# Optimization experiments

Hardware: AMD Instinct MI355X
Metric: run time of the kernel (lower is better)

## Reference

```python
import jax, jax.numpy as jnp
import numpy as np

B, T, C, H = 512, 256, 512, 4
HS = C // H          # head_size = 128
FF = 4 * C           # ffn_fanout * n_embd = 2048
NF = 2               # n_ffn dual FFN branches
EPS = 1e-8


def setup_inputs() -> dict:
    key = jax.random.key(0)
    ks = jax.random.split(key, 12)
    s = 0.02
    return {
        "x": jax.random.normal(ks[0], (B, T, C), jnp.float32),
        "Wq": jax.random.normal(ks[1], (H, C, HS), jnp.float32) * s,
        "Wk": jax.random.normal(ks[2], (H, C, HS), jnp.float32) * s,
        "bk": jax.random.normal(ks[3], (H, HS), jnp.float32) * s,
        "Wv": jax.random.normal(ks[4], (H, C, HS), jnp.float32) * s,
        "Wproj": jax.random.normal(ks[5], (C, C), jnp.float32) * s,
        "bproj": jax.random.normal(ks[6], (C,), jnp.float32) * s,
        "w1": jnp.ones((1,), jnp.float32),
        "w2": jnp.ones((1,), jnp.float32),
        "Wi": jax.random.normal(ks[7], (NF, C, FF), jnp.float32) * s,
        "Wo": jax.random.normal(ks[8], (NF, FF, C), jnp.float32) * s,
    }


def _rmsnorm(v, w):
    # MyNorm: scalar weight * x * rsqrt(mean(x^2, -1) + eps)
    return w * v * jax.lax.rsqrt(jnp.mean(v * v, axis=-1, keepdims=True) + EPS)


def reference(x, Wq, Wk, bk, Wv, Wproj, bproj, w1, w2, Wi, Wo):
    Bc, Tc, Cc = x.shape
    h = _rmsnorm(x, w1)
    # per-head projections (key has bias; query/value do not)
    q = jnp.einsum("btc,hcd->bhtd", h, Wq)
    k = jnp.einsum("btc,hcd->bhtd", h, Wk) + bk[None, :, None, :]
    v = jnp.einsum("btc,hcd->bhtd", h, Wv)
    # NOTE: original scales by full channel dim C**-0.5, not head_size
    scale = Cc ** (-0.5)
    wei = jnp.einsum("bhtd,bhsd->bhts", q, k) * scale
    causal = jnp.tril(jnp.ones((Tc, Tc), bool))
    wei = jnp.where(causal[None, None], wei, -jnp.inf)
    wei = jax.nn.softmax(wei, axis=-1)  # dropout: identity (inference)
    attn = jnp.einsum("bhts,bhsd->bhtd", wei, v)
    attn = attn.transpose(0, 2, 1, 3).reshape(Bc, Tc, Cc)
    x = x + attn @ Wproj + bproj  # dropout before proj: identity
    x = _rmsnorm(x, w2)
    # dual-branch FFN, averaged (exact GELU, as torch nn.GELU default)
    hmid = jax.nn.gelu(jnp.einsum("btc,ncf->nbtf", x, Wi), approximate=False)
    ff = jnp.mean(jnp.einsum("nbtf,nfc->nbtc", hmid, Wo), axis=0)
    return x + ff
```

## Files before the change

### kernel.cpp

```cpp
#include <hip/hip_runtime.h>
#include <cstdint>
#include <cstddef>

#define TOKENS 131072
#define B_BATCH 512
#define T_SEQ 256
#define C_DIM 512
#define H_HEADS 4
#define HS_DIM 128
#define FF_DIM 2048
#define EPS_RMS 1e-8f
#define SM_SCALE 0.044194173824159216f

typedef short bf16x8 __attribute__((ext_vector_type(8)));
typedef float f32x4 __attribute__((ext_vector_type(4)));
typedef unsigned short ushort_t;

__device__ __forceinline__ ushort_t f2bf(float f) {
    uint32_t u = __builtin_bit_cast(uint32_t, f);
    u += 0x7FFFu + ((u >> 16) & 1u);
    return (ushort_t)(u >> 16);
}

__device__ __forceinline__ float bf2f(ushort_t u) {
    return __builtin_bit_cast(float, (uint32_t)u << 16);
}

__device__ __forceinline__ float gelu_f(float x) {
    float u = 0.7978845608028654f * x + 0.035677408136300125f * (x * x * x);
    float e = __expf(2.0f * u);
    float t = 1.0f - 2.0f / (1.0f + e);
    return 0.5f * x * (1.0f + t);
}

__device__ __forceinline__ void stage8k(ushort_t* lds, const ushort_t* g) {
    __builtin_amdgcn_global_load_lds(
        (const __attribute__((address_space(1))) uint32_t*)g,
        (__attribute__((address_space(3))) uint32_t*)lds,
        16, 0, 0);
}

__global__ void prep_qkv(const float* __restrict__ Wq, const float* __restrict__ Wk,
                         const float* __restrict__ Wv, ushort_t* __restrict__ WqkvT) {
    int idx = blockIdx.x * 256 + threadIdx.x;
    if (idx >= 1536 * 512) return;
    int n = idx >> 9;
    int k = idx & 511;
    int h = (n & 511) >> 7;
    int d = n & 127;
    float v;
    size_t s = ((size_t)h * 512 + k) * 128 + d;
    if (n < 512)       v = Wq[s];
    else if (n < 1024) v = Wk[s];
    else               v = Wv[s];
    WqkvT[idx] = f2bf(v);
}

__global__ void prep_bias(const float* __restrict__ bk, float* __restrict__ bias1536) {
    int n = blockIdx.x * 256 + threadIdx.x;
    if (n >= 1536) return;
    bias1536[n] = (n >= 512 && n < 1024) ? bk[n - 512] : 0.0f;
}

__global__ void prep_proj(const float* __restrict__ Wproj, ushort_t* __restrict__ WprojT) {
    int idx = blockIdx.x * 256 + threadIdx.x;
    if (idx >= 512 * 512) return;
    int n = idx >> 9, k = idx & 511;
    WprojT[idx] = f2bf(Wproj[(size_t)k * 512 + n]);
}

__global__ void prep_wi(const float* __restrict__ Wi, ushort_t* __restrict__ WiT) {
    int idx = blockIdx.x * 256 + threadIdx.x;
    if (idx >= 2 * 2048 * 512) return;
    int b = idx >> 20;
    int rem = idx & 1048575;
    int f = rem >> 9, c = rem & 511;
    WiT[idx] = f2bf(Wi[((size_t)b * 512 + c) * 2048 + f]);
}

__global__ void prep_wo(const float* __restrict__ Wo, ushort_t* __restrict__ WoT2) {
    int idx = blockIdx.x * 256 + threadIdx.x;
    if (idx >= 512 * 4096) return;
    int c  = idx >> 12;
    int n2 = idx & 4095;
    int br = n2 >> 11;
    int f  = n2 & 2047;
    WoT2[idx] = f2bf(0.5f * Wo[(((size_t)br * 2048 + f) * 512) + c]);
}

__global__ __launch_bounds__(256) void rmsnorm_kernel(const float* __restrict__ in,
                                                      const float* __restrict__ wptr,
                                                      ushort_t* __restrict__ outb) {
    const int lane = threadIdx.x & 63;
    const int wave = threadIdx.x >> 6;
    const size_t token = (size_t)blockIdx.x * 4 + wave;
    const float* row = in + token * 512;
    float4 v0 = *(const float4*)(row + lane * 8);
    float4 v1 = *(const float4*)(row + lane * 8 + 4);
    float ss = v0.x*v0.x + v0.y*v0.y + v0.z*v0.z + v0.w*v0.w
             + v1.x*v1.x + v1.y*v1.y + v1.z*v1.z + v1.w*v1.w;
    #pragma unroll
    for (int d = 32; d; d >>= 1) ss += __shfl_xor(ss, d);
    float scale = wptr[0] * rsqrtf(ss * (1.0f / 512.0f) + EPS_RMS);
    float vals[8] = {v0.x, v0.y, v0.z, v0.w, v1.x, v1.y, v1.z, v1.w};
    union { ushort_t us[8]; uint4 u4; } pk;
    #pragma unroll
    for (int i = 0; i < 8; i++) pk.us[i] = f2bf(vals[i] * scale);
    *(uint4*)(outb + token * 512 + lane * 8) = pk.u4;
}

template<int MODE>
__global__ __launch_bounds__(512) void gemm256(
    const ushort_t* __restrict__ A, const ushort_t* __restrict__ Bt,
    float* Cf, ushort_t* __restrict__ Cb,
    const float* __restrict__ bias, const float* __restrict__ X,
    const ushort_t* __restrict__ Xb,
    int N, int K)
{
    __shared__ __align__(16) ushort_t S[2][2][256 * 64];
    const int tid  = threadIdx.x;
    const int lane = tid & 63;
    const int wave = tid >> 6;
    const int wm = wave >> 2;
    const int wn = wave & 3;

    const int nwg  = (int)gridDim.x;
    const int orig = (int)blockIdx.x;
    const int wgid = (orig & 7) * (nwg >> 3) + (orig >> 3);
    const int gx   = N >> 8;
    const int bm = (wgid / gx) << 8;
    const int bn = (wgid % gx) << 8;

    const int NT = K >> 6;

    const int sx = (((lane & 7) ^ (lane >> 3)) << 3);

    auto stA = [&](int dbuf, int part, int ts) {
        int tc = ts < NT ? ts : NT - 1;
        #pragma unroll
        for (int i = 0; i < 2; i++) {
            int rbase = i * 128 + part * 64 + wave * 8;
            stage8k(&S[dbuf][0][rbase * 64],
                    A + (size_t)(bm + rbase + (lane >> 3)) * K + tc * 64 + sx);
        }
    };
    auto stB = [&](int dbuf, int part, int ts) {
        int tc = ts < NT ? ts : NT - 1;
        #pragma unroll
        for (int i = 0; i < 2; i++) {
            int rbase = i * 128 + (wave >> 2) * 64 + part * 32 + (wave & 3) * 8;
            stage8k(&S[dbuf][1][rbase * 64],
                    Bt + (size_t)(bn + rbase + (lane >> 3)) * K + tc * 64 + sx);
        }
    };

    const int r16 = lane & 15;
    const int l7  = lane & 7;
    const int q   = lane >> 4;
    const int ge0 = ((q)     ^ l7) << 3;
    const int ge1 = ((4 + q) ^ l7) << 3;

    f32x4 acc[8][4] = {};
    bf16x8 a[4][2], bA[2][2], bB[2][2];

#define LDA(BUF, MH) { _Pragma("unroll") for (int mf = 0; mf < 4; mf++) { \
    int R = wm * 128 + (MH) * 64 + mf * 16 + r16; \
    a[mf][0] = *(const bf16x8*)&S[BUF][0][R * 64 + ge0]; \
    a[mf][1] = *(const bf16x8*)&S[BUF][0][R * 64 + ge1]; } }
#define LDB(BUF, NH, breg) { _Pragma("unroll") for (int nf = 0; nf < 2; nf++) { \
    int R = wn * 64 + (NH) * 32 + nf * 16 + r16; \
    breg[nf][0] = *(const bf16x8*)&S[BUF][1][R * 64 + ge0]; \
    breg[nf][1] = *(const bf16x8*)&S[BUF][1][R * 64 + ge1]; } }
#define MM(MH, NH, breg) { __builtin_amdgcn_s_setprio(1); \
    _Pragma("unroll") for (int mf = 0; mf < 4; mf++) \
    _Pragma("unroll") for (int nf = 0; nf < 2; nf++) { \
        f32x4 t0 = __builtin_amdgcn_mfma_f32_16x16x32_bf16(a[mf][0], breg[nf][0], acc[(MH)*4+mf][(NH)*2+nf], 0, 0, 0); \
        acc[(MH)*4+mf][(NH)*2+nf] = __builtin_amdgcn_mfma_f32_16x16x32_bf16(a[mf][1], breg[nf][1], t0, 0, 0, 0); } \
    __builtin_amdgcn_s_setprio(0); }
#define BAR    __builtin_amdgcn_s_barrier()
#define WAITL  { asm volatile("s_waitcnt lgkmcnt(0)" ::: "memory"); __builtin_amdgcn_sched_barrier(0); }
#define WAITLV { asm volatile("s_waitcnt lgkmcnt(0)\n\ts_waitcnt vmcnt(6)" ::: "memory"); __builtin_amdgcn_sched_barrier(0); }

    stA(0, 0, 0); stB(0, 0, 0); stB(0, 1, 0); stA(0, 1, 0);
    stA(1, 0, 1); stB(1, 0, 1); stB(1, 1, 1);
    asm volatile("s_waitcnt vmcnt(6)" ::: "memory");
    __builtin_amdgcn_sched_barrier(0);
    BAR;

    const int NI = NT >> 1;
    for (int I = 0; I < NI; ++I) {
        const int t = 2 * I;
        LDA(0, 0); LDB(0, 0, bA);  stA(1, 1, t + 1);  BAR; WAITL;  MM(0, 0, bA); BAR;
        LDB(0, 1, bB);             stA(0, 0, t + 2);  BAR; WAITL;  MM(0, 1, bB); BAR;
        LDA(0, 1);                 stB(0, 0, t + 2);  BAR; WAITL;  MM(1, 1, bB); BAR;
                                   stB(0, 1, t + 2);  BAR; WAITLV; MM(1, 0, bA); BAR;
        LDA(1, 0); LDB(1, 0, bA);  stA(0, 1, t + 2);  BAR; WAITL;  MM(0, 0, bA); BAR;
        LDB(1, 1, bB);             stA(1, 0, t + 3);  BAR; WAITL;  MM(0, 1, bB); BAR;
        LDA(1, 1);                 stB(1, 0, t + 3);  BAR; WAITL;  MM(1, 1, bB); BAR;
                                   stB(1, 1, t + 3);  BAR; WAITLV; MM(1, 0, bA); BAR;
    }
#undef LDA
#undef LDB
#undef MM
#undef BAR
#undef WAITL
#undef WAITLV

    #pragma unroll
    for (int mf = 0; mf < 8; mf++) {
        #pragma unroll
        for (int nf = 0; nf < 4; nf++) {
            #pragma unroll
            for (int j = 0; j < 4; j++) {
                int r = bm + wm * 128 + mf * 16 + (lane >> 4) * 4 + j;
                int c = bn + wn * 64 + nf * 16 + r16;
                float v = acc[mf][nf][j];
                size_t idx = (size_t)r * N + c;
                if (MODE == 0)      { Cb[idx] = f2bf(v + bias[c]); }
                else if (MODE == 1) { Cf[idx] = v + bias[c] + X[idx]; }
                else if (MODE == 2) { Cb[idx] = f2bf(gelu_f(v)); }
                else                { Cf[idx] = bf2f(Xb[idx]) + v; }
            }
        }
    }
}

__global__ __launch_bounds__(256) void attn_kernel(const ushort_t* __restrict__ QKV,
                                                   ushort_t* __restrict__ Ao) {
    __shared__ __align__(16) ushort_t Ks[32 * 136];
    __shared__ __align__(16) ushort_t VsT[128 * 40];
    __shared__ __align__(16) ushort_t Ps[4][16 * 40];
    const int tid  = threadIdx.x;
    const int lane = tid & 63;
    const int wave = tid >> 6;
    const int qtile = blockIdx.x;
    const int bh = blockIdx.y;
    const int b = bh >> 2;
    const int h = bh & 3;
    const int qb = qtile * 64;
    const int q0 = qb + wave * 16;
    const size_t baseTok = (size_t)b * T_SEQ;

    bf16x8 qf[4];
    {
        const ushort_t* qrow = QKV + (baseTok + q0 + (lane & 15)) * 1536 + h * 128 + (lane >> 4) * 8;
        #pragma unroll
        for (int dc = 0; dc < 4; dc++)
            qf[dc] = *(const bf16x8*)(qrow + dc * 32);
    }

    float m_run[4], l_run[4];
    f32x4 o[8];
    #pragma unroll
    for (int j = 0; j < 4; j++) { m_run[j] = -INFINITY; l_run[j] = 0.0f; }
    #pragma unroll
    for (int nt = 0; nt < 8; nt++) o[nt] = f32x4{0.f, 0.f, 0.f, 0.f};

    const int nchunks = qtile * 2 + 2;
    for (int kc = 0; kc < nchunks; kc++) {
        const int kbase = kc * 32;
        __syncthreads();
        #pragma unroll
        for (int r = 0; r < 2; r++) {
            int li = r * 256 + tid;
            int row = li >> 4;
            int c8 = (li & 15) * 8;
            size_t g = (baseTok + kbase + row) * 1536;
            uint4 vk = *(const uint4*)(QKV + g + 512 + h * 128 + c8);
            *(uint4*)(&Ks[row * 136 + c8]) = vk;
            uint4 vv = *(const uint4*)(QKV + g + 1024 + h * 128 + c8);
            ushort_t* pv = (ushort_t*)&vv;
            #pragma unroll
            for (int jj = 0; jj < 8; jj++)
                VsT[(c8 + jj) * 40 + row] = pv[jj];
        }
        __syncthreads();

        if (q0 + 15 >= kbase) {
            f32x4 s0 = {0.f,0.f,0.f,0.f}, s1 = {0.f,0.f,0.f,0.f};
            #pragma unroll
            for (int dc = 0; dc < 4; dc++) {
                bf16x8 kf0 = *(const bf16x8*)(&Ks[(lane & 15) * 136 + dc * 32 + (lane >> 4) * 8]);
                bf16x8 kf1 = *(const bf16x8*)(&Ks[(16 + (lane & 15)) * 136 + dc * 32 + (lane >> 4) * 8]);
                s0 = __builtin_amdgcn_mfma_f32_16x16x32_bf16(qf[dc], kf0, s0, 0, 0, 0);
                s1 = __builtin_amdgcn_mfma_f32_16x16x32_bf16(qf[dc], kf1, s1, 0, 0, 0);
            }
            const int key0 = kbase + (lane & 15);
            const int key1 = key0 + 16;
            float p0[4], p1[4], alpha[4];
            #pragma unroll
            for (int j = 0; j < 4; j++) {
                int qrow = q0 + (lane >> 4) * 4 + j;
                float sv0 = (key0 <= qrow) ? s0[j] * SM_SCALE : -INFINITY;
                float sv1 = (key1 <= qrow) ? s1[j] * SM_SCALE : -INFINITY;
                float mx = fmaxf(sv0, sv1);
                #pragma unroll
                for (int d = 1; d < 16; d <<= 1) mx = fmaxf(mx, __shfl_xor(mx, d));
                float mnew = fmaxf(m_run[j], mx);
                float aa = expf(m_run[j] - mnew);
                p0[j] = expf(sv0 - mnew);
                p1[j] = expf(sv1 - mnew);
                float rs = p0[j] + p1[j];
                #pragma unroll
                for (int d = 1; d < 16; d <<= 1) rs += __shfl_xor(rs, d);
                l_run[j] = l_run[j] * aa + rs;
                m_run[j] = mnew;
                alpha[j] = aa;
            }
            #pragma unroll
            for (int nt = 0; nt < 8; nt++)
                #pragma unroll
                for (int j = 0; j < 4; j++) o[nt][j] *= alpha[j];
            #pragma unroll
            for (int j = 0; j < 4; j++) {
                int rloc = (lane >> 4) * 4 + j;
                Ps[wave][rloc * 40 + (lane & 15)]      = f2bf(p0[j]);
                Ps[wave][rloc * 40 + 16 + (lane & 15)] = f2bf(p1[j]);
            }
            bf16x8 pa = *(const bf16x8*)(&Ps[wave][(lane & 15) * 40 + (lane >> 4) * 8]);
            #pragma unroll
            for (int nt = 0; nt < 8; nt++) {
                bf16x8 vf = *(const bf16x8*)(&VsT[(nt * 16 + (lane & 15)) * 40 + (lane >> 4) * 8]);
                o[nt] = __builtin_amdgcn_mfma_f32_16x16x32_bf16(pa, vf, o[nt], 0, 0, 0);
            }
        }
    }

    #pragma unroll
    for (int j = 0; j < 4; j++) {
        float inv = 1.0f / l_run[j];
        size_t row = baseTok + q0 + (lane >> 4) * 4 + j;
        #pragma unroll
        for (int nt = 0; nt < 8; nt++)
            Ao[row * 512 + h * 128 + nt * 16 + (lane & 15)] = f2bf(o[nt][j] * inv);
    }
}

extern "C" void kernel_launch(void* const* d_in, const int* in_sizes, int n_in,
                              void* d_out, int out_size, void* d_ws, size_t ws_size,
                              hipStream_t stream) {
    const float* x     = (const float*)d_in[0];
    const float* Wq    = (const float*)d_in[1];
    const float* Wk    = (const float*)d_in[2];
    const float* bk    = (const float*)d_in[3];
    const float* Wv    = (const float*)d_in[4];
    const float* Wproj = (const float*)d_in[5];
    const float* bproj = (const float*)d_in[6];
    const float* w1    = (const float*)d_in[7];
    const float* w2    = (const float*)d_in[8];
    const float* Wi    = (const float*)d_in[9];
    const float* Wo    = (const float*)d_in[10];
    float* out = (float*)d_out;
    (void)in_sizes; (void)n_in; (void)out_size;

    char* ws = (char*)d_ws;
    size_t off = 0;
    auto alloc = [&](size_t bytes) -> void* {
        void* p = ws + off;
        off += (bytes + 255) & ~(size_t)255;
        return p;
    };
    ushort_t* WqkvT    = (ushort_t*)alloc((size_t)1536 * 512 * 2);
    float*    bias1536 = (float*)   alloc((size_t)1536 * 4);
    ushort_t* WprojT   = (ushort_t*)alloc((size_t)512 * 512 * 2);
    ushort_t* WiT      = (ushort_t*)alloc((size_t)4096 * 512 * 2);
    ushort_t* WoT2     = (ushort_t*)alloc((size_t)512 * 4096 * 2);
    const size_t weightBytes = off;

    int nchunks = 1;
    while (nchunks < 64) {
        size_t Mc = (size_t)TOKENS / nchunks;
        size_t need = weightBytes + Mc * 512 * 2 + Mc * 4096 * 2 + 4096;
        if (need <= ws_size) break;
        nchunks *= 2;
    }
    const size_t Mc = (size_t)TOKENS / nchunks;
    const int    nbChunk = B_BATCH / nchunks;

    ushort_t* hb  = (ushort_t*)alloc(Mc * 512 * 2);
    ushort_t* big = (ushort_t*)alloc(Mc * 4096 * 2);

    prep_qkv <<<(1536 * 512 + 255) / 256, 256, 0, stream>>>(Wq, Wk, Wv, WqkvT);
    prep_bias<<<6, 256, 0, stream>>>(bk, bias1536);
    prep_proj<<<1024, 256, 0, stream>>>(Wproj, WprojT);
    prep_wi  <<<8192, 256, 0, stream>>>(Wi, WiT);
    prep_wo  <<<8192, 256, 0, stream>>>(Wo, WoT2);

    for (int ck = 0; ck < nchunks; ck++) {
        const size_t t0 = (size_t)ck * Mc;
        const float* xC   = x + t0 * 512;
        float*       zC   = out + t0 * 512;
        const int    Mi   = (int)Mc;
        const int    mt   = Mi / 256;

        rmsnorm_kernel<<<Mi / 4, 256, 0, stream>>>(xC, w1, hb);
        gemm256<0><<<mt * 6, 512, 0, stream>>>(
            hb, WqkvT, nullptr, big, bias1536, nullptr, nullptr, 1536, 512);
        attn_kernel<<<dim3(T_SEQ / 64, nbChunk * H_HEADS), 256, 0, stream>>>(big, hb);
        gemm256<1><<<mt * 2, 512, 0, stream>>>(
            hb, WprojT, zC, nullptr, bproj, xC, nullptr, 512, 512);
        rmsnorm_kernel<<<Mi / 4, 256, 0, stream>>>(zC, w2, hb);
        gemm256<2><<<mt * 16, 512, 0, stream>>>(
            hb, WiT, nullptr, big, nullptr, nullptr, nullptr, 4096, 512);
        gemm256<3><<<mt * 2, 512, 0, stream>>>(
            big, WoT2, zC, nullptr, nullptr, nullptr, hb, 512, 4096);
    }
}
```

Baseline: 2.479 ms.

## Replace 256x256 ping-pong GEMM with 128x128 triple-buffered GEMM

Swaps the 512-thread 256x256 tile GEMM, which used a hand-interleaved double-buffered schedule, for a 256-thread 128x128 tile kernel with K-step 32 and a three-stage LDS ring buffer. The grids are doubled or quadrupled to match. The simpler pipeline keeps two stages in flight and adds more workgroups, which may improve occupancy and load balance. The cost is lower arithmetic intensity per tile, more global traffic, and one barrier per K-step.

Measured after the change: 2.967 ms. 1.2x slower.

```diff
diff --git a/kernel.cpp b/kernel.cpp
--- a/kernel.cpp
+++ b/kernel.cpp
@@ -110,109 +110,88 @@
 }
 
 template<int MODE>
-__global__ __launch_bounds__(512) void gemm256(
+__global__ __launch_bounds__(256) void gemm128(
     const ushort_t* __restrict__ A, const ushort_t* __restrict__ Bt,
     float* Cf, ushort_t* __restrict__ Cb,
     const float* __restrict__ bias, const float* __restrict__ X,
     const ushort_t* __restrict__ Xb,
     int N, int K)
 {
-    __shared__ __align__(16) ushort_t S[2][2][256 * 64];
+    __shared__ __align__(16) ushort_t S[3][2][128 * 32];
     const int tid  = threadIdx.x;
     const int lane = tid & 63;
     const int wave = tid >> 6;
-    const int wm = wave >> 2;
-    const int wn = wave & 3;
+    const int wm = wave >> 1;
+    const int wn = wave & 1;
 
     const int nwg  = (int)gridDim.x;
     const int orig = (int)blockIdx.x;
     const int wgid = (orig & 7) * (nwg >> 3) + (orig >> 3);
-    const int gx   = N >> 8;
-    const int bm = (wgid / gx) << 8;
-    const int bn = (wgid % gx) << 8;
-
-    const int NT = K >> 6;
-
-    const int sx = (((lane & 7) ^ (lane >> 3)) << 3);
-
-    auto stA = [&](int dbuf, int part, int ts) {
+    const int gx   = N >> 7;
+    const int bm = (wgid / gx) << 7;
+    const int bn = (wgid % gx) << 7;
+
+    const int NT = K >> 5;
+
+    const int srcg = (((lane & 3) ^ ((lane >> 4) & 3)) << 3);
+
+    auto stage = [&](int sb, int ts) {
         int tc = ts < NT ? ts : NT - 1;
+        const int ko = tc << 5;
         #pragma unroll
         for (int i = 0; i < 2; i++) {
-            int rbase = i * 128 + part * 64 + wave * 8;
-            stage8k(&S[dbuf][0][rbase * 64],
-                    A + (size_t)(bm + rbase + (lane >> 3)) * K + tc * 64 + sx);
+            const int rb = (wave * 2 + i) * 16;
+            stage8k(&S[sb][0][rb * 32],
+                    A + (size_t)(bm + rb + (lane >> 2)) * K + ko + srcg);
+            stage8k(&S[sb][1][rb * 32],
+                    Bt + (size_t)(bn + rb + (lane >> 2)) * K + ko + srcg);
         }
     };
-    auto stB = [&](int dbuf, int part, int ts) {
-        int tc = ts < NT ? ts : NT - 1;
-        #pragma unroll
-        for (int i = 0; i < 2; i++) {
-            int rbase = i * 128 + (wave >> 2) * 64 + part * 32 + (wave & 3) * 8;
-            stage8k(&S[dbuf][1][rbase * 64],
-                    Bt + (size_t)(bn + rbase + (lane >> 3)) * K + tc * 64 + sx);
-        }
-    };
 
     const int r16 = lane & 15;
-    const int l7  = lane & 7;
     const int q   = lane >> 4;
-    const int ge0 = ((q)     ^ l7) << 3;
-    const int ge1 = ((4 + q) ^ l7) << 3;
-
-    f32x4 acc[8][4] = {};
-    bf16x8 a[4][2], bA[2][2], bB[2][2];
-
-#define LDA(BUF, MH) { _Pragma("unroll") for (int mf = 0; mf < 4; mf++) { \
-    int R = wm * 128 + (MH) * 64 + mf * 16 + r16; \
-    a[mf][0] = *(const bf16x8*)&S[BUF][0][R * 64 + ge0]; \
-    a[mf][1] = *(const bf16x8*)&S[BUF][0][R * 64 + ge1]; } }
-#define LDB(BUF, NH, breg) { _Pragma("unroll") for (int nf = 0; nf < 2; nf++) { \
-    int R = wn * 64 + (NH) * 32 + nf * 16 + r16; \
-    breg[nf][0] = *(const bf16x8*)&S[BUF][1][R * 64 + ge0]; \
-    breg[nf][1] = *(const bf16x8*)&S[BUF][1][R * 64 + ge1]; } }
-#define MM(MH, NH, breg) { __builtin_amdgcn_s_setprio(1); \
-    _Pragma("unroll") for (int mf = 0; mf < 4; mf++) \
-    _Pragma("unroll") for (int nf = 0; nf < 2; nf++) { \
-        f32x4 t0 = __builtin_amdgcn_mfma_f32_16x16x32_bf16(a[mf][0], breg[nf][0], acc[(MH)*4+mf][(NH)*2+nf], 0, 0, 0); \
-        acc[(MH)*4+mf][(NH)*2+nf] = __builtin_amdgcn_mfma_f32_16x16x32_bf16(a[mf][1], breg[nf][1], t0, 0, 0, 0); } \
-    __builtin_amdgcn_s_setprio(0); }
-#define BAR    __builtin_amdgcn_s_barrier()
-#define WAITL  { asm volatile("s_waitcnt lgkmcnt(0)" ::: "memory"); __builtin_amdgcn_sched_barrier(0); }
-#define WAITLV { asm volatile("s_waitcnt lgkmcnt(0)\n\ts_waitcnt vmcnt(6)" ::: "memory"); __builtin_amdgcn_sched_barrier(0); }
-
-    stA(0, 0, 0); stB(0, 0, 0); stB(0, 1, 0); stA(0, 1, 0);
-    stA(1, 0, 1); stB(1, 0, 1); stB(1, 1, 1);
-    asm volatile("s_waitcnt vmcnt(6)" ::: "memory");
-    __builtin_amdgcn_sched_barrier(0);
-    BAR;
-
-    const int NI = NT >> 1;
-    for (int I = 0; I < NI; ++I) {
-        const int t = 2 * I;
-        LDA(0, 0); LDB(0, 0, bA);  stA(1, 1, t + 1);  BAR; WAITL;  MM(0, 0, bA); BAR;
-        LDB(0, 1, bB);             stA(0, 0, t + 2);  BAR; WAITL;  MM(0, 1, bB); BAR;
-        LDA(0, 1);                 stB(0, 0, t + 2);  BAR; WAITL;  MM(1, 1, bB); BAR;
-                                   stB(0, 1, t + 2);  BAR; WAITLV; MM(1, 0, bA); BAR;
-        LDA(1, 0); LDB(1, 0, bA);  stA(0, 1, t + 2);  BAR; WAITL;  MM(0, 0, bA); BAR;
-        LDB(1, 1, bB);             stA(1, 0, t + 3);  BAR; WAITL;  MM(0, 1, bB); BAR;
-        LDA(1, 1);                 stB(1, 0, t + 3);  BAR; WAITL;  MM(1, 1, bB); BAR;
-                                   stB(1, 1, t + 3);  BAR; WAITLV; MM(1, 0, bA); BAR;
-    }
-#undef LDA
-#undef LDB
-#undef MM
-#undef BAR
-#undef WAITL
-#undef WAITLV
-
-    #pragma unroll
-    for (int mf = 0; mf < 8; mf++) {
+    const int ge  = ((q ^ ((r16 >> 2) & 3)) << 3);
+    const int aBase = (wm * 64 + r16) * 32 + ge;
+    const int bBase = (wn * 64 + r16) * 32 + ge;
+
+    f32x4 acc[4][4] = {};
+    bf16x8 af[4], bf[4];
+
+    stage(0, 0);
+    stage(1, 1);
+    asm volatile("s_waitcnt vmcnt(4)" ::: "memory");
+    __builtin_amdgcn_s_barrier();
+
+    int cur = 0;
+    for (int t = 0; t < NT; ++t) {
+        int nxt = cur + 2; if (nxt >= 3) nxt -= 3;
+        stage(nxt, t + 2);
+        #pragma unroll
+        for (int mf = 0; mf < 4; mf++)
+            af[mf] = *(const bf16x8*)&S[cur][0][aBase + mf * 512];
+        #pragma unroll
+        for (int nf = 0; nf < 4; nf++)
+            bf[nf] = *(const bf16x8*)&S[cur][1][bBase + nf * 512];
+        __builtin_amdgcn_s_setprio(1);
+        #pragma unroll
+        for (int mf = 0; mf < 4; mf++)
+            #pragma unroll
+            for (int nf = 0; nf < 4; nf++)
+                acc[mf][nf] = __builtin_amdgcn_mfma_f32_16x16x32_bf16(
+                    af[mf], bf[nf], acc[mf][nf], 0, 0, 0);
+        __builtin_amdgcn_s_setprio(0);
+        asm volatile("s_waitcnt lgkmcnt(0)\n\ts_waitcnt vmcnt(4)" ::: "memory");
+        __builtin_amdgcn_s_barrier();
+        cur = (cur == 2) ? 0 : cur + 1;
+    }
+
+    #pragma unroll
+    for (int mf = 0; mf < 4; mf++) {
         #pragma unroll
         for (int nf = 0; nf < 4; nf++) {
             #pragma unroll
             for (int j = 0; j < 4; j++) {
-                int r = bm + wm * 128 + mf * 16 + (lane >> 4) * 4 + j;
+                int r = bm + wm * 64 + mf * 16 + q * 4 + j;
                 int c = bn + wn * 64 + nf * 16 + r16;
                 float v = acc[mf][nf][j];
                 size_t idx = (size_t)r * N + c;
@@ -391,18 +370,18 @@
         const float* xC   = x + t0 * 512;
         float*       zC   = out + t0 * 512;
         const int    Mi   = (int)Mc;
-        const int    mt   = Mi / 256;
+        const int    mt   = Mi / 128;
 
         rmsnorm_kernel<<<Mi / 4, 256, 0, stream>>>(xC, w1, hb);
-        gemm256<0><<<mt * 6, 512, 0, stream>>>(
+        gemm128<0><<<mt * 12, 256, 0, stream>>>(
             hb, WqkvT, nullptr, big, bias1536, nullptr, nullptr, 1536, 512);
         attn_kernel<<<dim3(T_SEQ / 64, nbChunk * H_HEADS), 256, 0, stream>>>(big, hb);
-        gemm256<1><<<mt * 2, 512, 0, stream>>>(
+        gemm128<1><<<mt * 4, 256, 0, stream>>>(
             hb, WprojT, zC, nullptr, bproj, xC, nullptr, 512, 512);
         rmsnorm_kernel<<<Mi / 4, 256, 0, stream>>>(zC, w2, hb);
-        gemm256<2><<<mt * 16, 512, 0, stream>>>(
+        gemm128<2><<<mt * 32, 256, 0, stream>>>(
             hb, WiT, nullptr, big, nullptr, nullptr, nullptr, 4096, 512);
-        gemm256<3><<<mt * 2, 512, 0, stream>>>(
+        gemm128<3><<<mt * 4, 256, 0, stream>>>(
             big, WoT2, zC, nullptr, nullptr, nullptr, hb, 512, 4096);
     }
 }
```
